# Kernel optimization log

Measured on AMD Instinct MI355X. Metric: run time of the kernel, lower is better.

## Reference

```python
import jax, jax.numpy as jnp
import numpy as np

B, D, S = 8, 128, 4096

def setup_inputs() -> dict:
    key = jax.random.key(0)
    ks = jax.random.split(key, 7)
    sd = 1.0 / np.sqrt(D)
    return {
        "x": jax.random.normal(ks[0], (B, D, S), dtype=jnp.float32),
        "Wq": jax.random.normal(ks[1], (D, D), dtype=jnp.float32) * sd,
        "bq": jax.random.normal(ks[2], (D,), dtype=jnp.float32) * sd,
        "Wk": jax.random.normal(ks[3], (D, D), dtype=jnp.float32) * sd,
        "bk": jax.random.normal(ks[4], (D,), dtype=jnp.float32) * sd,
        "Wv": jax.random.normal(ks[5], (D, D), dtype=jnp.float32) * sd,
        "bv": jax.random.normal(ks[6], (D,), dtype=jnp.float32) * sd,
    }

def reference(x, Wq, bq, Wk, bk, Wv, bv):
    # x: (B, D, S) -> (B, S, D)
    xt = jnp.transpose(x, (0, 2, 1))
    scale = jnp.asarray(D, xt.dtype) ** 0.5
    # torch Linear: y = x @ W.T + b
    Q = jnp.einsum('bsd,ed->bse', xt, Wq) + bq
    K = jnp.einsum('bsd,ed->bse', xt, Wk) + bk
    V = jnp.einsum('bsd,ed->bse', xt, Wv) + bv
    scores = jnp.einsum('bqd,bkd->bqk', Q, K) / scale  # (B, S, S)
    attn = jax.nn.softmax(scores, axis=-1)
    attended = jnp.einsum('bqk,bkd->bqd', attn, V)
    out = xt + attended  # residual
    return jnp.transpose(out, (0, 2, 1))  # back to (B, D, S)
```

## Files before the change

### kernel.cpp

```cpp
#include <hip/hip_runtime.h>
#include <hip/hip_bf16.h>

#define B_ 8
#define D_ 128
#define S_ 4096

typedef short short8 __attribute__((ext_vector_type(8)));
typedef float f32x4  __attribute__((ext_vector_type(4)));
typedef float f32x16 __attribute__((ext_vector_type(16)));
typedef unsigned int uint;
typedef uint uint4v __attribute__((ext_vector_type(4)));

#define EXP2F(x) exp2f(x)

__device__ __forceinline__ short f2bf(float f) {
    __hip_bfloat16 h = __float2bfloat16(f);
    return *reinterpret_cast<short*>(&h);
}

__device__ __forceinline__ uint cvtpk(float lo, float hi) {
    uint r;
    asm("v_cvt_pk_bf16_f32 %0, %1, %2" : "=v"(r) : "v"(lo), "v"(hi));
    return r;
}

__device__ __forceinline__ void gload16(const void* g, void* l) {
    __builtin_amdgcn_global_load_lds(
        (const __attribute__((address_space(1))) void*)g,
        (__attribute__((address_space(3))) void*)l, 16, 0, 0);
}

__global__ __launch_bounds__(256) void wpack_kernel(
    const float* __restrict__ Wq, const float* __restrict__ Wk,
    const float* __restrict__ Wv, short* __restrict__ Wf)
{
    int g = blockIdx.x * 256 + threadIdx.x;
    int lane = g & 63, kc = (g >> 6) & 3, n = (g >> 8) & 7, wm = g >> 11;
    const float* W = (wm == 0) ? Wq : (wm == 1) ? Wk : Wv;
    int row = n * 16 + (lane & 15);
    int col = kc * 32 + (lane >> 4) * 8;
    short8 o;
    #pragma unroll
    for (int j = 0; j < 8; ++j) o[j] = f2bf(W[row * 128 + col + j]);
    *((short8*)Wf + g) = o;
}

__global__ __launch_bounds__(256) void qkv_kernel(
    const float* __restrict__ x, const short* __restrict__ Wf,
    const float* __restrict__ bq, const float* __restrict__ bk,
    const float* __restrict__ bv,
    short* __restrict__ Qo, short* __restrict__ Ko, short* __restrict__ Vo)
{
    __shared__ float xt[64 * 132];
    const int b  = blockIdx.y;
    const int s0 = blockIdx.x * 64;
    const int t  = threadIdx.x;
    const int w    = t >> 6;
    const int lane = t & 63;
    const int lr   = lane & 15;
    const int lg   = lane >> 4;

    const float* xb = x + (size_t)b * D_ * S_;
    #pragma unroll
    for (int it = 0; it < 32; ++it) {
        int d = it * 4 + (t >> 6);
        int s = t & 63;
        xt[s * 132 + d] = xb[(size_t)d * S_ + s0 + s];
    }
    __syncthreads();

    short8 xtf[4];
    {
        const float* base = &xt[(w * 16 + lr) * 132 + lg * 8];
        #pragma unroll
        for (int kc = 0; kc < 4; ++kc) {
            float4 a = *(const float4*)(base + kc * 32);
            float4 c = *(const float4*)(base + kc * 32 + 4);
            short8 f;
            f[0] = f2bf(a.x); f[1] = f2bf(a.y); f[2] = f2bf(a.z); f[3] = f2bf(a.w);
            f[4] = f2bf(c.x); f[5] = f2bf(c.y); f[6] = f2bf(c.z); f[7] = f2bf(c.w);
            xtf[kc] = f;
        }
    }

    const float qs = 0.08838834764831845f * 1.4426950408889634f;
    const short8* W8 = (const short8*)Wf;
    const size_t bSD = (size_t)b * S_ * D_;
    const size_t bDS = (size_t)b * D_ * S_;

    #pragma unroll
    for (int n = 0; n < 8; ++n) {
        f32x4 aq = (f32x4){0.f, 0.f, 0.f, 0.f};
        f32x4 ak = (f32x4){0.f, 0.f, 0.f, 0.f};
        f32x4 av = (f32x4){0.f, 0.f, 0.f, 0.f};
        #pragma unroll
        for (int kc = 0; kc < 4; ++kc) {
            short8 wq = W8[(      n * 4 + kc) * 64 + lane];
            short8 wk = W8[(32  + n * 4 + kc) * 64 + lane];
            short8 wv = W8[(64  + n * 4 + kc) * 64 + lane];
            aq = __builtin_amdgcn_mfma_f32_16x16x32_bf16(xtf[kc], wq, aq, 0, 0, 0);
            ak = __builtin_amdgcn_mfma_f32_16x16x32_bf16(xtf[kc], wk, ak, 0, 0, 0);
            av = __builtin_amdgcn_mfma_f32_16x16x32_bf16(wv, xtf[kc], av, 0, 0, 0);
        }
        int e = n * 16 + lr;
        float bqe = bq[e], bke = bk[e];
        #pragma unroll
        for (int r = 0; r < 4; ++r) {
            size_t off = (bSD + (size_t)(s0 + w * 16 + lg * 4 + r) * D_) + e;
            Qo[off] = f2bf((aq[r] + bqe) * qs);
            Ko[off] = f2bf(ak[r] + bke);
        }
        #pragma unroll
        for (int r = 0; r < 4; ++r) {
            int ev = n * 16 + lg * 4 + r;
            Vo[bDS + (size_t)ev * S_ + s0 + w * 16 + lr] = f2bf(av[r] + bv[ev]);
        }
    }
}

__global__ __launch_bounds__(512, 2) void attn_kernel(
    const short* __restrict__ Q, const short* __restrict__ K,
    const short* __restrict__ Vt, const float* __restrict__ x,
    float* __restrict__ out)
{
    extern __shared__ __align__(16) char smem[];
    const int lin = blockIdx.x;
    const int b   = lin & 7;
    const int q0  = (lin >> 3) * 128;
    const int tid  = threadIdx.x;
    const int w    = tid >> 6;
    const int lane = tid & 63;
    const int q    = lane & 31;
    const int hi   = lane >> 5;
    const int half = w >> 2;
    const int ww   = w & 3;

    const size_t bSD = (size_t)b * S_ * D_;

    short8 qf[8];
    {
        const short* Qrow = Q + bSD + (size_t)(q0 + ww * 32 + q) * D_ + hi * 8;
        #pragma unroll
        for (int c = 0; c < 8; ++c)
            qf[c] = *(const short8*)(Qrow + c * 16);
    }

    f32x16 o[4];
    #pragma unroll
    for (int dt = 0; dt < 4; ++dt)
        #pragma unroll
        for (int i = 0; i < 16; ++i) o[dt][i] = 0.f;
    float m = -1e30f, lsum = 0.f;

    const short* Kb = K + bSD;
    const short* Vb = Vt + (size_t)b * D_ * S_;
    const int ktbase = half * 32;

    char* const Kd0 = smem + half * 65536;
    char* const Kd1 = Kd0 + 16384;
    char* const Vd0 = Kd0 + 32768;
    char* const Vd1 = Vd0 + 16384;

    auto stageK = [&](int kt, char* Kd) {
        const short* Kg = Kb + (size_t)(ktbase + kt) * 64 * D_;
        #pragma unroll
        for (int i = 0; i < 4; ++i) {
            int ki = ww * 4 + i;
            int r  = ki * 4 + (lane >> 4);
            gload16(Kg + r * D_ + (((lane & 15) ^ (r & 7)) * 8), Kd + ki * 1024);
        }
    };
    auto stageV = [&](int kt, char* Vd) {
        const short* Vg = Vb + (size_t)(ktbase + kt) * 64;
        #pragma unroll
        for (int i = 0; i < 4; ++i) {
            int vi = ww * 4 + i;
            int r  = vi * 8 + (lane >> 3);
            gload16(Vg + (size_t)r * S_ + (((lane & 7) ^ (lane >> 3)) * 8),
                    Vd + vi * 1024);
        }
    };

    auto qkrun = [&](const char* Kh, f32x16& a0, f32x16& a1) {
        #pragma unroll
        for (int i = 0; i < 16; ++i) { a0[i] = 0.f; a1[i] = 0.f; }
        __builtin_amdgcn_s_setprio(1);
        #pragma unroll
        for (int c = 0; c < 8; ++c) {
            int co = ((c * 2 + hi) ^ (q & 7)) * 16;
            short8 k0 = *(const short8*)(Kh + q * 256 + co);
            short8 k1 = *(const short8*)(Kh + (32 + q) * 256 + co);
            a0 = __builtin_amdgcn_mfma_f32_32x32x16_bf16(k0, qf[c], a0, 0, 0, 0);
            a1 = __builtin_amdgcn_mfma_f32_32x32x16_bf16(k1, qf[c], a1, 0, 0, 0);
        }
        __builtin_amdgcn_s_setprio(0);
    };

    auto body = [&](int t, char* KstD, char* VstD, const char* Krd,
                    const char* Vrd, f32x16& iA0, f32x16& iA1,
                    f32x16& oB0, f32x16& oB1) {
        if (t + 2 < 32) stageK(t + 2, KstD);
        if (t + 1 < 32) stageV(t + 1, VstD);

        float x0 = fmaxf(fmaxf(iA0[0],  iA0[1]),  fmaxf(iA0[2],  iA0[3]));
        float x1 = fmaxf(fmaxf(iA0[4],  iA0[5]),  fmaxf(iA0[6],  iA0[7]));
        float x2 = fmaxf(fmaxf(iA0[8],  iA0[9]),  fmaxf(iA0[10], iA0[11]));
        float x3 = fmaxf(fmaxf(iA0[12], iA0[13]), fmaxf(iA0[14], iA0[15]));
        float x4 = fmaxf(fmaxf(iA1[0],  iA1[1]),  fmaxf(iA1[2],  iA1[3]));
        float x5 = fmaxf(fmaxf(iA1[4],  iA1[5]),  fmaxf(iA1[6],  iA1[7]));
        float x6 = fmaxf(fmaxf(iA1[8],  iA1[9]),  fmaxf(iA1[10], iA1[11]));
        float x7 = fmaxf(fmaxf(iA1[12], iA1[13]), fmaxf(iA1[14], iA1[15]));
        float tm = fmaxf(fmaxf(fmaxf(x0, x1), fmaxf(x2, x3)),
                         fmaxf(fmaxf(x4, x5), fmaxf(x6, x7)));
        tm = fmaxf(tm, __shfl_xor(tm, 32));
        if (!__all(tm <= m + 8.f)) {
            float mn   = fmaxf(m, tm);
            float corr = EXP2F(m - mn);
            m = mn; lsum *= corr;
            #pragma unroll
            for (int dt = 0; dt < 4; ++dt)
                #pragma unroll
                for (int r = 0; r < 16; ++r) o[dt][r] *= corr;
        }

        if (t + 1 < 32) qkrun(Krd, oB0, oB1);

        #pragma unroll
        for (int r = 0; r < 16; ++r) iA0[r] = EXP2F(iA0[r] - m);
        #pragma unroll
        for (int r = 0; r < 16; ++r) iA1[r] = EXP2F(iA1[r] - m);
        float s0 = ((iA0[0]+iA0[1])+(iA0[2]+iA0[3]))
                 + ((iA0[4]+iA0[5])+(iA0[6]+iA0[7]));
        float s1 = ((iA0[8]+iA0[9])+(iA0[10]+iA0[11]))
                 + ((iA0[12]+iA0[13])+(iA0[14]+iA0[15]));
        float s2 = ((iA1[0]+iA1[1])+(iA1[2]+iA1[3]))
                 + ((iA1[4]+iA1[5])+(iA1[6]+iA1[7]));
        float s3 = ((iA1[8]+iA1[9])+(iA1[10]+iA1[11]))
                 + ((iA1[12]+iA1[13])+(iA1[14]+iA1[15]));
        float ps = (s0 + s1) + (s2 + s3);
        ps += __shfl_xor(ps, 32);
        lsum += ps;

        short8 pf[4];
        #pragma unroll
        for (int kc = 0; kc < 4; ++kc) {
            const f32x16& a = (kc < 2) ? iA0 : iA1;
            int c1 = (kc & 1) * 8;
            uint W0 = cvtpk(a[c1 + 0], a[c1 + 1]);
            uint W1 = cvtpk(a[c1 + 2], a[c1 + 3]);
            uint W2 = cvtpk(a[c1 + 4], a[c1 + 5]);
            uint W3 = cvtpk(a[c1 + 6], a[c1 + 7]);
            asm("v_permlane32_swap_b32 %0, %1" : "+v"(W0), "+v"(W2));
            asm("v_permlane32_swap_b32 %0, %1" : "+v"(W1), "+v"(W3));
            uint4v pw;
            pw.x = W0; pw.y = W1; pw.z = W2; pw.w = W3;
            pf[kc] = *reinterpret_cast<short8*>(&pw);
        }

        __builtin_amdgcn_s_setprio(1);
        #pragma unroll
        for (int kc = 0; kc < 4; ++kc)
            #pragma unroll
            for (int dt = 0; dt < 4; ++dt) {
                int row = dt * 32 + q;
                short8 vf = *(const short8*)(Vrd + row * 128
                              + (((kc * 2 + hi) ^ (q & 7)) * 16));
                o[dt] = __builtin_amdgcn_mfma_f32_32x32x16_bf16(vf, pf[kc], o[dt], 0, 0, 0);
            }
        __builtin_amdgcn_s_setprio(0);

        __syncthreads();
    };

    stageK(0, Kd0); stageV(0, Vd0); stageK(1, Kd1);
    __syncthreads();
    f32x16 aA0, aA1, aB0, aB1;
    #pragma unroll
    for (int i = 0; i < 16; ++i) { aB0[i] = 0.f; aB1[i] = 0.f; }
    qkrun(Kd0, aA0, aA1);
    __syncthreads();

    for (int t = 0; t < 32; t += 2) {
        body(t,     Kd0, Vd1, Kd1, Vd0, aA0, aA1, aB0, aB1);
        body(t + 1, Kd1, Vd0, Kd0, Vd1, aB0, aB1, aA0, aA1);
    }

    if (half == 1) {
        float* obuf = (float*)(smem + ww * 16384);
        #pragma unroll
        for (int dt = 0; dt < 4; ++dt)
            #pragma unroll
            for (int r = 0; r < 16; ++r) {
                int dl = dt * 32 + (r & 3) + 8 * (r >> 2) + 4 * hi;
                obuf[dl * 32 + q] = o[dt][r];
            }
        if (hi == 0) {
            float* ml = (float*)(smem + 65536 + ww * 256);
            ml[q * 2]     = m;
            ml[q * 2 + 1] = lsum;
        }
    }
    __syncthreads();
    if (half == 0) {
        const float* obuf = (const float*)(smem + ww * 16384);
        const float* ml   = (const float*)(smem + 65536 + ww * 256);
        float m2 = ml[q * 2], l2 = ml[q * 2 + 1];
        float M  = fmaxf(m, m2);
        float c1 = EXP2F(m - M), c2 = EXP2F(m2 - M);
        float inv = 1.0f / (lsum * c1 + l2 * c2);
        const float* xb = x   + (size_t)b * D_ * S_;
        float*       ob = out + (size_t)b * D_ * S_;
        int s = q0 + ww * 32 + q;
        #pragma unroll
        for (int dt = 0; dt < 4; ++dt)
            #pragma unroll
            for (int r = 0; r < 16; ++r) {
                int dl = dt * 32 + (r & 3) + 8 * (r >> 2) + 4 * hi;
                float val = (o[dt][r] * c1 + obuf[dl * 32 + q] * c2) * inv;
                size_t g = (size_t)dl * S_ + s;
                ob[g] = xb[g] + val;
            }
    }
}

extern "C" void kernel_launch(void* const* d_in, const int* in_sizes, int n_in,
                              void* d_out, int out_size, void* d_ws, size_t ws_size,
                              hipStream_t stream) {
    const float* x  = (const float*)d_in[0];
    const float* Wq = (const float*)d_in[1];
    const float* bq = (const float*)d_in[2];
    const float* Wk = (const float*)d_in[3];
    const float* bk = (const float*)d_in[4];
    const float* Wv = (const float*)d_in[5];
    const float* bv = (const float*)d_in[6];
    float* out = (float*)d_out;

    size_t n = (size_t)B_ * S_ * D_;
    short* Qw = (short*)d_ws;
    short* Kw = Qw + n;
    short* Vw = Kw + n;
    short* Wf = (short*)d_out;

    wpack_kernel<<<24, 256, 0, stream>>>(Wq, Wk, Wv, Wf);

    dim3 grid(S_ / 64, B_);
    qkv_kernel<<<grid, 256, 0, stream>>>(x, Wf, bq, bk, bv, Qw, Kw, Vw);

    int smemB = 131072;
    (void)hipFuncSetAttribute((const void*)attn_kernel,
                              hipFuncAttributeMaxDynamicSharedMemorySize, smemB);
    attn_kernel<<<256, 512, smemB, stream>>>(Qw, Kw, Vw, x, out);
}
```

Before: 123.8 us.

## Give each wave two 32-row query tiles, halve block threads, drop software-pipelined QK

The attention kernel now runs 256 threads per block (4 waves) instead of 512, and each wave handles 64 query rows as two 32-row groups that share each K and V fragment read from LDS. The intent is to halve LDS traffic per MFMA and amortise K/V staging over more compute. The QK-ahead software pipelining and s_setprio hints are removed in favour of a simple double-buffered loop, and each wave now holds double the register state. Occupancy falls to one 4-wave block per CU, with LDS grown slightly for the m/l exchange, which risks latency exposure since softmax no longer overlaps with MFMA.

```diff
diff --git a/kernel.cpp b/kernel.cpp
--- a/kernel.cpp
+++ b/kernel.cpp
@@ -118,7 +118,7 @@
     }
 }
 
-__global__ __launch_bounds__(512, 2) void attn_kernel(
+__global__ __launch_bounds__(256, 1) void attn_kernel(
     const short* __restrict__ Q, const short* __restrict__ K,
     const short* __restrict__ Vt, const float* __restrict__ x,
     float* __restrict__ out)
@@ -132,84 +132,68 @@
     const int lane = tid & 63;
     const int q    = lane & 31;
     const int hi   = lane >> 5;
-    const int half = w >> 2;
-    const int ww   = w & 3;
+    const int half = w >> 1;
+    const int ww   = w & 1;
 
     const size_t bSD = (size_t)b * S_ * D_;
 
-    short8 qf[8];
+    short8 qf0[8], qf1[8];
     {
-        const short* Qrow = Q + bSD + (size_t)(q0 + ww * 32 + q) * D_ + hi * 8;
-        #pragma unroll
-        for (int c = 0; c < 8; ++c)
-            qf[c] = *(const short8*)(Qrow + c * 16);
-    }
-
-    f32x16 o[4];
+        const short* Qr0 = Q + bSD + (size_t)(q0 + ww * 64 + q) * D_ + hi * 8;
+        const short* Qr1 = Qr0 + 32 * D_;
+        #pragma unroll
+        for (int c = 0; c < 8; ++c) {
+            qf0[c] = *(const short8*)(Qr0 + c * 16);
+            qf1[c] = *(const short8*)(Qr1 + c * 16);
+        }
+    }
+
+    f32x16 o0[4], o1[4];
     #pragma unroll
     for (int dt = 0; dt < 4; ++dt)
         #pragma unroll
-        for (int i = 0; i < 16; ++i) o[dt][i] = 0.f;
-    float m = -1e30f, lsum = 0.f;
+        for (int i = 0; i < 16; ++i) { o0[dt][i] = 0.f; o1[dt][i] = 0.f; }
+    float m0 = -1e30f, l0 = 0.f, m1 = -1e30f, l1 = 0.f;
 
     const short* Kb = K + bSD;
     const short* Vb = Vt + (size_t)b * D_ * S_;
-    const int ktbase = half * 32;
-
-    char* const Kd0 = smem + half * 65536;
-    char* const Kd1 = Kd0 + 16384;
-    char* const Vd0 = Kd0 + 32768;
-    char* const Vd1 = Vd0 + 16384;
-
-    auto stageK = [&](int kt, char* Kd) {
-        const short* Kg = Kb + (size_t)(ktbase + kt) * 64 * D_;
-        #pragma unroll
-        for (int i = 0; i < 4; ++i) {
-            int ki = ww * 4 + i;
+    const int kvbase = half * 2048;
+
+    char* const Kbase = smem + half * 65536;
+    char* const Vbase = Kbase + 32768;
+
+    auto stageK = [&](int kt, int buf) {
+        const short* Kg = Kb + (size_t)(kvbase + kt * 64) * D_;
+        char* Kd = Kbase + buf * 16384;
+        #pragma unroll
+        for (int i = 0; i < 8; ++i) {
+            int ki = ww * 8 + i;
             int r  = ki * 4 + (lane >> 4);
             gload16(Kg + r * D_ + (((lane & 15) ^ (r & 7)) * 8), Kd + ki * 1024);
         }
     };
-    auto stageV = [&](int kt, char* Vd) {
-        const short* Vg = Vb + (size_t)(ktbase + kt) * 64;
-        #pragma unroll
-        for (int i = 0; i < 4; ++i) {
-            int vi = ww * 4 + i;
+    auto stageV = [&](int kt, int buf) {
+        const short* Vg = Vb + kvbase + kt * 64;
+        char* Vd = Vbase + buf * 16384;
+        #pragma unroll
+        for (int i = 0; i < 8; ++i) {
+            int vi = ww * 8 + i;
             int r  = vi * 8 + (lane >> 3);
             gload16(Vg + (size_t)r * S_ + (((lane & 7) ^ (lane >> 3)) * 8),
                     Vd + vi * 1024);
         }
     };
 
-    auto qkrun = [&](const char* Kh, f32x16& a0, f32x16& a1) {
-        #pragma unroll
-        for (int i = 0; i < 16; ++i) { a0[i] = 0.f; a1[i] = 0.f; }
-        __builtin_amdgcn_s_setprio(1);
-        #pragma unroll
-        for (int c = 0; c < 8; ++c) {
-            int co = ((c * 2 + hi) ^ (q & 7)) * 16;
-            short8 k0 = *(const short8*)(Kh + q * 256 + co);
-            short8 k1 = *(const short8*)(Kh + (32 + q) * 256 + co);
-            a0 = __builtin_amdgcn_mfma_f32_32x32x16_bf16(k0, qf[c], a0, 0, 0, 0);
-            a1 = __builtin_amdgcn_mfma_f32_32x32x16_bf16(k1, qf[c], a1, 0, 0, 0);
-        }
-        __builtin_amdgcn_s_setprio(0);
-    };
-
-    auto body = [&](int t, char* KstD, char* VstD, const char* Krd,
-                    const char* Vrd, f32x16& iA0, f32x16& iA1,
-                    f32x16& oB0, f32x16& oB1) {
-        if (t + 2 < 32) stageK(t + 2, KstD);
-        if (t + 1 < 32) stageV(t + 1, VstD);
-
-        float x0 = fmaxf(fmaxf(iA0[0],  iA0[1]),  fmaxf(iA0[2],  iA0[3]));
-        float x1 = fmaxf(fmaxf(iA0[4],  iA0[5]),  fmaxf(iA0[6],  iA0[7]));
-        float x2 = fmaxf(fmaxf(iA0[8],  iA0[9]),  fmaxf(iA0[10], iA0[11]));
-        float x3 = fmaxf(fmaxf(iA0[12], iA0[13]), fmaxf(iA0[14], iA0[15]));
-        float x4 = fmaxf(fmaxf(iA1[0],  iA1[1]),  fmaxf(iA1[2],  iA1[3]));
-        float x5 = fmaxf(fmaxf(iA1[4],  iA1[5]),  fmaxf(iA1[6],  iA1[7]));
-        float x6 = fmaxf(fmaxf(iA1[8],  iA1[9]),  fmaxf(iA1[10], iA1[11]));
-        float x7 = fmaxf(fmaxf(iA1[12], iA1[13]), fmaxf(iA1[14], iA1[15]));
+    auto smqb = [&](f32x16& A0, f32x16& A1, float& m, float& lsum,
+                    f32x16* o, short8* pf) {
+        float x0 = fmaxf(fmaxf(A0[0],  A0[1]),  fmaxf(A0[2],  A0[3]));
+        float x1 = fmaxf(fmaxf(A0[4],  A0[5]),  fmaxf(A0[6],  A0[7]));
+        float x2 = fmaxf(fmaxf(A0[8],  A0[9]),  fmaxf(A0[10], A0[11]));
+        float x3 = fmaxf(fmaxf(A0[12], A0[13]), fmaxf(A0[14], A0[15]));
+        float x4 = fmaxf(fmaxf(A1[0],  A1[1]),  fmaxf(A1[2],  A1[3]));
+        float x5 = fmaxf(fmaxf(A1[4],  A1[5]),  fmaxf(A1[6],  A1[7]));
+        float x6 = fmaxf(fmaxf(A1[8],  A1[9]),  fmaxf(A1[10], A1[11]));
+        float x7 = fmaxf(fmaxf(A1[12], A1[13]), fmaxf(A1[14], A1[15]));
         float tm = fmaxf(fmaxf(fmaxf(x0, x1), fmaxf(x2, x3)),
                          fmaxf(fmaxf(x4, x5), fmaxf(x6, x7)));
         tm = fmaxf(tm, __shfl_xor(tm, 32));
@@ -222,29 +206,21 @@
                 #pragma unroll
                 for (int r = 0; r < 16; ++r) o[dt][r] *= corr;
         }
-
-        if (t + 1 < 32) qkrun(Krd, oB0, oB1);
-
-        #pragma unroll
-        for (int r = 0; r < 16; ++r) iA0[r] = EXP2F(iA0[r] - m);
-        #pragma unroll
-        for (int r = 0; r < 16; ++r) iA1[r] = EXP2F(iA1[r] - m);
-        float s0 = ((iA0[0]+iA0[1])+(iA0[2]+iA0[3]))
-                 + ((iA0[4]+iA0[5])+(iA0[6]+iA0[7]));
-        float s1 = ((iA0[8]+iA0[9])+(iA0[10]+iA0[11]))
-                 + ((iA0[12]+iA0[13])+(iA0[14]+iA0[15]));
-        float s2 = ((iA1[0]+iA1[1])+(iA1[2]+iA1[3]))
-                 + ((iA1[4]+iA1[5])+(iA1[6]+iA1[7]));
-        float s3 = ((iA1[8]+iA1[9])+(iA1[10]+iA1[11]))
-                 + ((iA1[12]+iA1[13])+(iA1[14]+iA1[15]));
+        #pragma unroll
+        for (int r = 0; r < 16; ++r) A0[r] = EXP2F(A0[r] - m);
+        #pragma unroll
+        for (int r = 0; r < 16; ++r) A1[r] = EXP2F(A1[r] - m);
+        float s0 = ((A0[0]+A0[1])+(A0[2]+A0[3])) + ((A0[4]+A0[5])+(A0[6]+A0[7]));
+        float s1 = ((A0[8]+A0[9])+(A0[10]+A0[11])) + ((A0[12]+A0[13])+(A0[14]+A0[15]));
+        float s2 = ((A1[0]+A1[1])+(A1[2]+A1[3])) + ((A1[4]+A1[5])+(A1[6]+A1[7]));
+        float s3 = ((A1[8]+A1[9])+(A1[10]+A1[11])) + ((A1[12]+A1[13])+(A1[14]+A1[15]));
         float ps = (s0 + s1) + (s2 + s3);
         ps += __shfl_xor(ps, 32);
         lsum += ps;
 
-        short8 pf[4];
         #pragma unroll
         for (int kc = 0; kc < 4; ++kc) {
-            const f32x16& a = (kc < 2) ? iA0 : iA1;
+            const f32x16& a = (kc < 2) ? A0 : A1;
             int c1 = (kc & 1) * 8;
             uint W0 = cvtpk(a[c1 + 0], a[c1 + 1]);
             uint W1 = cvtpk(a[c1 + 2], a[c1 + 3]);
@@ -256,70 +232,112 @@
             pw.x = W0; pw.y = W1; pw.z = W2; pw.w = W3;
             pf[kc] = *reinterpret_cast<short8*>(&pw);
         }
-
-        __builtin_amdgcn_s_setprio(1);
+    };
+
+    auto tilebody = [&](int buf) {
+        const char* Kh = Kbase + buf * 16384;
+        const char* Vh = Vbase + buf * 16384;
+
+        f32x16 a00, a01, a10, a11;
+        #pragma unroll
+        for (int i = 0; i < 16; ++i) { a00[i]=0.f; a01[i]=0.f; a10[i]=0.f; a11[i]=0.f; }
+        #pragma unroll
+        for (int c = 0; c < 8; ++c) {
+            int co = ((c * 2 + hi) ^ (q & 7)) * 16;
+            short8 k0 = *(const short8*)(Kh + q * 256 + co);
+            short8 k1 = *(const short8*)(Kh + (32 + q) * 256 + co);
+            a00 = __builtin_amdgcn_mfma_f32_32x32x16_bf16(k0, qf0[c], a00, 0, 0, 0);
+            a01 = __builtin_amdgcn_mfma_f32_32x32x16_bf16(k1, qf0[c], a01, 0, 0, 0);
+            a10 = __builtin_amdgcn_mfma_f32_32x32x16_bf16(k0, qf1[c], a10, 0, 0, 0);
+            a11 = __builtin_amdgcn_mfma_f32_32x32x16_bf16(k1, qf1[c], a11, 0, 0, 0);
+        }
+
+        short8 pf0[4], pf1[4];
+        smqb(a00, a01, m0, l0, o0, pf0);
+        smqb(a10, a11, m1, l1, o1, pf1);
+
         #pragma unroll
         for (int kc = 0; kc < 4; ++kc)
             #pragma unroll
             for (int dt = 0; dt < 4; ++dt) {
                 int row = dt * 32 + q;
-                short8 vf = *(const short8*)(Vrd + row * 128
+                short8 vf = *(const short8*)(Vh + row * 128
                               + (((kc * 2 + hi) ^ (q & 7)) * 16));
-                o[dt] = __builtin_amdgcn_mfma_f32_32x32x16_bf16(vf, pf[kc], o[dt], 0, 0, 0);
+                o0[dt] = __builtin_amdgcn_mfma_f32_32x32x16_bf16(vf, pf0[kc], o0[dt], 0, 0, 0);
+                o1[dt] = __builtin_amdgcn_mfma_f32_32x32x16_bf16(vf, pf1[kc], o1[dt], 0, 0, 0);
             }
-        __builtin_amdgcn_s_setprio(0);
-
+    };
+
+    stageK(0, 0); stageV(0, 0);
+    __syncthreads();
+    int cur = 0;
+
+    for (int kt = 0; kt < 31; ++kt) {
+        stageK(kt + 1, cur ^ 1);
+        stageV(kt + 1, cur ^ 1);
+        tilebody(cur);
         __syncthreads();
-    };
-
-    stageK(0, Kd0); stageV(0, Vd0); stageK(1, Kd1);
+        cur ^= 1;
+    }
+    tilebody(cur);
+
     __syncthreads();
-    f32x16 aA0, aA1, aB0, aB1;
-    #pragma unroll
-    for (int i = 0; i < 16; ++i) { aB0[i] = 0.f; aB1[i] = 0.f; }
-    qkrun(Kd0, aA0, aA1);
-    __syncthreads();
-
-    for (int t = 0; t < 32; t += 2) {
-        body(t,     Kd0, Vd1, Kd1, Vd0, aA0, aA1, aB0, aB1);
-        body(t + 1, Kd1, Vd0, Kd0, Vd1, aB0, aB1, aA0, aA1);
-    }
-
+    float2* ml = (float2*)(smem + 131072);
     if (half == 1) {
-        float* obuf = (float*)(smem + ww * 16384);
+        float* obuf = (float*)(smem + ww * 32768);
         #pragma unroll
         for (int dt = 0; dt < 4; ++dt)
             #pragma unroll
             for (int r = 0; r < 16; ++r) {
                 int dl = dt * 32 + (r & 3) + 8 * (r >> 2) + 4 * hi;
-                obuf[dl * 32 + q] = o[dt][r];
+                obuf[dl * 64 + q]      = o0[dt][r];
+                obuf[dl * 64 + 32 + q] = o1[dt][r];
             }
         if (hi == 0) {
-            float* ml = (float*)(smem + 65536 + ww * 256);
-            ml[q * 2]     = m;
-            ml[q * 2 + 1] = lsum;
+            float2 v0; v0.x = m0; v0.y = l0;
+            float2 v1; v1.x = m1; v1.y = l1;
+            ml[ww * 64 + q]      = v0;
+            ml[ww * 64 + 32 + q] = v1;
         }
     }
     __syncthreads();
     if (half == 0) {
-        const float* obuf = (const float*)(smem + ww * 16384);
-        const float* ml   = (const float*)(smem + 65536 + ww * 256);
-        float m2 = ml[q * 2], l2 = ml[q * 2 + 1];
-        float M  = fmaxf(m, m2);
-        float c1 = EXP2F(m - M), c2 = EXP2F(m2 - M);
-        float inv = 1.0f / (lsum * c1 + l2 * c2);
+        const float* obuf = (const float*)(smem + ww * 32768);
         const float* xb = x   + (size_t)b * D_ * S_;
         float*       ob = out + (size_t)b * D_ * S_;
-        int s = q0 + ww * 32 + q;
-        #pragma unroll
-        for (int dt = 0; dt < 4; ++dt)
-            #pragma unroll
-            for (int r = 0; r < 16; ++r) {
-                int dl = dt * 32 + (r & 3) + 8 * (r >> 2) + 4 * hi;
-                float val = (o[dt][r] * c1 + obuf[dl * 32 + q] * c2) * inv;
-                size_t g = (size_t)dl * S_ + s;
-                ob[g] = xb[g] + val;
-            }
+
+        float2 p0 = ml[ww * 64 + q];
+        float2 p1 = ml[ww * 64 + 32 + q];
+        {
+            float M  = fmaxf(m0, p0.x);
+            float c1 = EXP2F(m0 - M), c2 = EXP2F(p0.x - M);
+            float inv = 1.0f / (l0 * c1 + p0.y * c2);
+            int s = q0 + ww * 64 + q;
+            #pragma unroll
+            for (int dt = 0; dt < 4; ++dt)
+                #pragma unroll
+                for (int r = 0; r < 16; ++r) {
+                    int dl = dt * 32 + (r & 3) + 8 * (r >> 2) + 4 * hi;
+                    float val = (o0[dt][r] * c1 + obuf[dl * 64 + q] * c2) * inv;
+                    size_t g = (size_t)dl * S_ + s;
+                    ob[g] = xb[g] + val;
+                }
+        }
+        {
+            float M  = fmaxf(m1, p1.x);
+            float c1 = EXP2F(m1 - M), c2 = EXP2F(p1.x - M);
+            float inv = 1.0f / (l1 * c1 + p1.y * c2);
+            int s = q0 + ww * 64 + 32 + q;
+            #pragma unroll
+            for (int dt = 0; dt < 4; ++dt)
+                #pragma unroll
+                for (int r = 0; r < 16; ++r) {
+                    int dl = dt * 32 + (r & 3) + 8 * (r >> 2) + 4 * hi;
+                    float val = (o1[dt][r] * c1 + obuf[dl * 64 + 32 + q] * c2) * inv;
+                    size_t g = (size_t)dl * S_ + s;
+                    ob[g] = xb[g] + val;
+                }
+        }
     }
 }
 
@@ -346,8 +364,8 @@
     dim3 grid(S_ / 64, B_);
     qkv_kernel<<<grid, 256, 0, stream>>>(x, Wf, bq, bk, bv, Qw, Kw, Vw);
 
-    int smemB = 131072;
+    int smemB = 132096;
     (void)hipFuncSetAttribute((const void*)attn_kernel,
                               hipFuncAttributeMaxDynamicSharedMemorySize, smemB);
-    attn_kernel<<<256, 512, smemB, stream>>>(Qw, Kw, Vw, x, out);
-}
+    attn_kernel<<<256, 256, smemB, stream>>>(Qw, Kw, Vw, x, out);
+}
```

After: 142.2 us. 1.15x slower.
